# Performance work log

Hardware: AMD Instinct MI355X
Metric: run time of the kernel (lower is better)

The kernel has to match this reference:

```python
import jax, jax.numpy as jnp
import numpy as np

B, T, C = 2, 2048, 1024
NH = 16
HD = C // NH

def build_alibi_bias(n_head, max_len):
    slopes = jnp.arange(1, n_head + 1, dtype=jnp.float32) / n_head  # [nh]
    ar = jnp.arange(max_len, dtype=jnp.float32)
    # bias[h, i, j] = slopes[h] * (j - i)
    return slopes[:, None, None] * (ar[None, None, :] - ar[None, :, None])

def setup_inputs() -> dict:
    key = jax.random.key(0)
    ks = jax.random.split(key, 7)
    s = 0.02
    return {
        "x": jax.random.normal(ks[0], (B, T, C), dtype=jnp.float32),
        "q_w": jax.random.normal(ks[1], (C, C), dtype=jnp.float32) * s,   # [in, out]
        "q_b": jnp.zeros((C,), dtype=jnp.float32),
        "kv_w": jax.random.normal(ks[2], (C, 2 * C), dtype=jnp.float32) * s,
        "kv_b": jnp.zeros((2 * C,), dtype=jnp.float32),
        "o_w": jax.random.normal(ks[3], (C, C), dtype=jnp.float32) * s,
        "o_b": jnp.zeros((C,), dtype=jnp.float32),
    }

def reference(x, q_w, q_b, kv_w, kv_b, o_w, o_b):
    Bx, Tx, Cx = x.shape
    q = (x @ q_w + q_b).reshape(Bx, Tx, NH, HD).transpose(0, 2, 1, 3)      # [B,nh,T,hd]
    kv = (x @ kv_w + kv_b).reshape(Bx, Tx, 2, NH, HD).transpose(2, 0, 3, 1, 4)
    k, v = kv[0], kv[1]                                                     # [B,nh,T,hd]
    att = jnp.einsum("bhqd,bhkd->bhqk", q, k) * (1.0 / np.sqrt(HD))        # [B,nh,T,T]
    att = att + build_alibi_bias(NH, Tx)[None]                              # ALiBi bias
    causal = jnp.tril(jnp.ones((Tx, Tx), dtype=bool))
    att = jnp.where(causal[None, None], att, -jnp.inf)
    att = jax.nn.softmax(att, axis=-1)
    y = jnp.einsum("bhqk,bhkd->bhqd", att, v)                               # [B,nh,T,hd]
    y = y.transpose(0, 2, 1, 3).reshape(Bx, Tx, Cx)
    return y @ o_w + o_b
```

## Files before the change

kernel.cpp:

```cpp
#include <hip/hip_runtime.h>
#include <hip/hip_bf16.h>

#define NB 2
#define NT 2048
#define NC 1024
#define NHD 16
#define HDD 64
#define LOG2E 1.4426950408889634f

typedef __attribute__((ext_vector_type(8))) short short8;
typedef __attribute__((ext_vector_type(4))) short short4v;
typedef __attribute__((ext_vector_type(4))) float f32x4;
typedef __attribute__((ext_vector_type(16))) float f32x16;

__device__ __forceinline__ ushort f2bf(float f) {
    union { float f; unsigned u; } v; v.f = f;
    unsigned u = v.u;
    unsigned r = (u + 0x7FFFu + ((u >> 16) & 1u)) >> 16;
    return (ushort)r;
}

__device__ __forceinline__ float bf2f(ushort u) {
    unsigned x = ((unsigned)u) << 16;
    float f; __builtin_memcpy(&f, &x, 4); return f;
}

__device__ __forceinline__ unsigned pkbf(float a, float b) {
    __hip_bfloat162 t = __float22bfloat162_rn(float2{a, b});
    unsigned u; __builtin_memcpy(&u, &t, 4); return u;
}

__device__ __forceinline__ void gload16(const ushort* g, ushort* l) {
    __builtin_amdgcn_global_load_lds((const __attribute__((address_space(1))) void*)g,
                                     (__attribute__((address_space(3))) void*)l, 16, 0, 0);
}

__device__ __forceinline__ void tcvt_tile(const float* __restrict__ src, ushort* __restrict__ dst,
                                          int Kd, int Nd, int kb, int nb)
{
    __shared__ ushort tile[64][68];
    const int tid = threadIdx.x;
    const int r = tid >> 2, c = (tid & 3) * 16;
    const float* sp = src + (size_t)(kb + r) * Nd + nb + c;
#pragma unroll
    for (int i = 0; i < 16; i += 4) {
        float4 v = *(const float4*)(sp + i);
        tile[r][c + i + 0] = f2bf(v.x);
        tile[r][c + i + 1] = f2bf(v.y);
        tile[r][c + i + 2] = f2bf(v.z);
        tile[r][c + i + 3] = f2bf(v.w);
    }
    __syncthreads();
    ushort* dp = dst + (size_t)(nb + r) * Kd + kb + c;
#pragma unroll
    for (int i = 0; i < 16; i += 8) {
        short8 o;
#pragma unroll
        for (int j = 0; j < 8; j++) o[j] = (short)tile[c + i + j][r];
        *(short8*)(dp + i) = o;
    }
}

__global__ __launch_bounds__(256)
void prep(const float* __restrict__ x, const float* __restrict__ q_w,
          const float* __restrict__ kv_w, const float* __restrict__ o_w,
          ushort* __restrict__ xb, ushort* __restrict__ wqkvT, ushort* __restrict__ woT)
{
    const int bid = blockIdx.x;
    if (bid < 2048) {
        int i = (bid * 256 + threadIdx.x) * 8;
        float4 a = *(const float4*)(x + i);
        float4 b = *(const float4*)(x + i + 4);
        short8 o;
        o[0] = (short)f2bf(a.x); o[1] = (short)f2bf(a.y);
        o[2] = (short)f2bf(a.z); o[3] = (short)f2bf(a.w);
        o[4] = (short)f2bf(b.x); o[5] = (short)f2bf(b.y);
        o[6] = (short)f2bf(b.z); o[7] = (short)f2bf(b.w);
        *(short8*)(xb + i) = o;
    } else if (bid < 2304) {
        int r = bid - 2048;
        tcvt_tile(q_w, wqkvT, 1024, 1024, (r & 15) * 64, (r >> 4) * 64);
    } else if (bid < 2816) {
        int r = bid - 2304;
        tcvt_tile(kv_w, wqkvT + 1024 * 1024, 1024, 2048, (r & 15) * 64, (r >> 4) * 64);
    } else {
        int r = bid - 2816;
        tcvt_tile(o_w, woT, 1024, 1024, (r & 15) * 64, (r >> 4) * 64);
    }
}

template<int MODE>
__global__ __launch_bounds__(256)
void gemm128(const ushort* __restrict__ A, const ushort* __restrict__ Bt,
             const float* __restrict__ bias0, const float* __restrict__ bias1,
             ushort* __restrict__ Qo, ushort* __restrict__ Ko, ushort* __restrict__ VoT,
             float* __restrict__ Fo, int Kdim)
{
    __shared__ ushort Al[2][128 * 32];
    __shared__ ushort Bl[2][128 * 32];
    const int tid = threadIdx.x;
    const int lane = tid & 63, w = tid >> 6;
    const int wr = (w >> 1) * 64, wc = (w & 1) * 64;
    const int lg = lane >> 4, lc = lane & 15;

    const int nwg = gridDim.x;
    const int cpx = nwg >> 3;
    const int sid = (blockIdx.x & 7) * cpx + (blockIdx.x >> 3);
    const int bm = (sid & 31) * 128, bn = (sid >> 5) * 128;

    f32x4 acc[4][4] = {};

    const int srow = lane >> 2, scol = (lane & 3) * 8;
    const int seg0 = w * 2;

    const ushort* apb = A  + (size_t)(bm + seg0 * 16 + srow) * Kdim + scol;
    const ushort* bpb = Bt + (size_t)(bn + seg0 * 16 + srow) * Kdim + scol;

    gload16(apb,              &Al[0][seg0 * 512]);
    gload16(apb + 16 * Kdim,  &Al[0][(seg0 + 1) * 512]);
    gload16(bpb,              &Bl[0][seg0 * 512]);
    gload16(bpb + 16 * Kdim,  &Bl[0][(seg0 + 1) * 512]);

    int cur = 0;
    for (int k0 = 0; k0 < Kdim; k0 += 32) {
        __syncthreads();
        if (k0 + 32 < Kdim) {
            gload16(apb + (k0 + 32),             &Al[cur ^ 1][seg0 * 512]);
            gload16(apb + (k0 + 32) + 16 * Kdim, &Al[cur ^ 1][(seg0 + 1) * 512]);
            gload16(bpb + (k0 + 32),             &Bl[cur ^ 1][seg0 * 512]);
            gload16(bpb + (k0 + 32) + 16 * Kdim, &Bl[cur ^ 1][(seg0 + 1) * 512]);
        }
        short8 af[4], bfv[4];
#pragma unroll
        for (int mt = 0; mt < 4; mt++) af[mt] = *(const short8*)&Al[cur][(wr + mt*16 + lc) * 32 + lg*8];
#pragma unroll
        for (int nt = 0; nt < 4; nt++) bfv[nt] = *(const short8*)&Bl[cur][(wc + nt*16 + lc) * 32 + lg*8];
        __builtin_amdgcn_s_setprio(1);
#pragma unroll
        for (int mt = 0; mt < 4; mt++)
#pragma unroll
            for (int nt = 0; nt < 4; nt++)
                acc[mt][nt] = __builtin_amdgcn_mfma_f32_16x16x32_bf16(af[mt], bfv[nt], acc[mt][nt], 0, 0, 0);
        __builtin_amdgcn_s_setprio(0);
        cur ^= 1;
    }

#pragma unroll
    for (int mt = 0; mt < 4; mt++) {
#pragma unroll
        for (int nt = 0; nt < 4; nt++) {
            const int n = bn + wc + nt * 16 + lc;
            const int mb = bm + wr + mt * 16 + lg * 4;
            if (MODE == 1) {
#pragma unroll
                for (int rr = 0; rr < 4; rr++)
                    Fo[(size_t)(mb + rr) * NC + n] = acc[mt][nt][rr] + bias0[n];
            } else {
                const int b = mb >> 11, t = mb & 2047;
                const int reg = n >> 10;
                if (reg == 0) {
                    int hh = n >> 6, d = n & 63;
                    ushort* qp = Qo + (((size_t)b * NHD + hh) * NT + t) * HDD + d;
#pragma unroll
                    for (int rr = 0; rr < 4; rr++)
                        qp[rr * HDD] = f2bf((acc[mt][nt][rr] + bias0[n]) * (0.125f * LOG2E));
                } else if (reg == 1) {
                    int j = n - NC;
                    int hh = j >> 6, d = j & 63;
                    ushort* kp = Ko + (((size_t)b * NHD + hh) * NT + t) * HDD + d;
#pragma unroll
                    for (int rr = 0; rr < 4; rr++)
                        kp[rr * HDD] = f2bf(acc[mt][nt][rr] + bias1[j]);
                } else {
                    int j = n - NC;
                    int jj = j - 1024;
                    int hh = jj >> 6, d = jj & 63;
                    short4v o;
#pragma unroll
                    for (int rr = 0; rr < 4; rr++)
                        o[rr] = (short)f2bf(acc[mt][nt][rr] + bias1[j]);
                    *(short4v*)&VoT[(((size_t)b * NHD + hh) * HDD + d) * NT + t] = o;
                }
            }
        }
    }
}

__global__ __launch_bounds__(256, 3)
void attn_fwd(const ushort* __restrict__ Q, const ushort* __restrict__ K,
              const ushort* __restrict__ Vt, ushort* __restrict__ Y,
              ushort* __restrict__ pool0, ushort* __restrict__ pool1,
              float* __restrict__ mlb)
{
    __shared__ ushort sb[2 * 2 * 64 * 72];

    const int tid = threadIdx.x;
    const int lane = tid & 63, w = tid >> 6;
    const int lo5 = lane & 31, hi = lane >> 5;
    const int slot = (int)(blockIdx.x >> 5);
    const int bh = blockIdx.x & 31;
    const int b = bh >> 4, h = bh & 15;

    int qt, seg, nseg;
    if (slot < 16)      { qt = 15 - (slot >> 2); seg = slot & 3; nseg = 4; }
    else if (slot < 28) { int u = slot - 16; int q3 = u / 3; qt = 11 - q3; seg = u - q3 * 3; nseg = 3; }
    else if (slot < 36) { int u = slot - 28; qt = 7 - (u >> 1); seg = u & 1; nseg = 2; }
    else                { qt = 39 - slot; seg = 0; nseg = 1; }
    const int T = 2 * qt + 2;
    const int t_begin = (seg * T) / nseg;
    const int t_end   = ((seg + 1) * T) / nseg;
    const bool split = (nseg > 1);
    int pi = 0;
    if (split) {
        int pbase = (qt < 8) ? (qt - 4) * 2 : ((qt < 12) ? 8 + (qt - 8) * 3 : 20 + (qt - 12) * 4);
        pi = bh * 36 + pbase + seg;
    }

    const ushort* Qp = Q + (size_t)bh * NT * HDD;
    const ushort* Kp = K + (size_t)bh * NT * HDD;
    const ushort* Vp = Vt + (size_t)bh * HDD * NT;

    const int q0 = qt * 128 + w * 32;
    const int qlane = q0 + lo5;

    const float slope2 = (float)(h + 1) * (LOG2E / (float)NHD);

    short8 qf[4];
    {
        const ushort* qr = Qp + (size_t)qlane * HDD + 8 * hi;
#pragma unroll
        for (int kk = 0; kk < 4; kk++) qf[kk] = *(const short8*)(qr + kk * 16);
    }

    short8 ones;
#pragma unroll
    for (int j = 0; j < 8; j++) ones[j] = (short)0x3F80;

    float bb[16];
#pragma unroll
    for (int r = 0; r < 16; r++) {
        int roff = (r & 3) + 8 * (r >> 2) + 4 * hi;
        bb[r] = slope2 * ((float)roff - (float)qlane);
    }

    float m_s = -1e30f, l_s = 0.f;
    f32x16 accO[2] = {};

    const int sr = tid >> 2, sd = (tid & 3) * 16;

    short8 pk0, pk1, pv0, pv1;
    {
        const ushort* kp = Kp + (size_t)(t_begin * 64 + sr) * HDD + sd;
        pk0 = *(const short8*)kp;
        pk1 = *(const short8*)(kp + 8);
        const ushort* vp = Vp + (size_t)sr * NT + t_begin * 64 + sd;
        pv0 = *(const short8*)vp;
        pv1 = *(const short8*)(vp + 8);
    }

    for (int t = t_begin; t < t_end; t++) {
        const int kv0 = t * 64;
        ushort* Kl = sb + ((t - t_begin) & 1) * 2 * 64 * 72;
        ushort* Vl = Kl + 64 * 72;
        *(short8*)&Kl[sr * 72 + sd]     = pk0;
        *(short8*)&Kl[sr * 72 + sd + 8] = pk1;
        *(short8*)&Vl[sr * 72 + sd]     = pv0;
        *(short8*)&Vl[sr * 72 + sd + 8] = pv1;
        __syncthreads();

        if (t + 1 < t_end) {
            const int kv1 = kv0 + 64;
            const ushort* kp = Kp + (size_t)(kv1 + sr) * HDD + sd;
            pk0 = *(const short8*)kp;
            pk1 = *(const short8*)(kp + 8);
            const ushort* vp = Vp + (size_t)sr * NT + kv1 + sd;
            pv0 = *(const short8*)vp;
            pv1 = *(const short8*)(vp + 8);
        }

#pragma unroll
        for (int sub = 0; sub < 2; sub++) {
            const int kv0s = kv0 + sub * 32;
            if (kv0s > q0 + 31) continue;

            f32x16 S = {};
            __builtin_amdgcn_s_setprio(1);
#pragma unroll
            for (int kk = 0; kk < 4; kk++) {
                short8 kf = *(const short8*)&Kl[(sub * 32 + lo5) * 72 + kk * 16 + 8 * hi];
                S = __builtin_amdgcn_mfma_f32_32x32x16_bf16(kf, qf[kk], S, 0, 0, 0);
            }
            __builtin_amdgcn_s_setprio(0);

            const float sk = slope2 * (float)kv0s;
            float mloc = m_s - sk;

            if (kv0s + 31 > q0) {
#pragma unroll
                for (int r = 0; r < 16; r++) {
                    int kvr = kv0s + (r & 3) + 8 * (r >> 2) + 4 * hi;
                    S[r] = (kvr > qlane) ? -1e30f : (S[r] + bb[r]);
                }
            } else {
#pragma unroll
                for (int r = 0; r < 16; r++) S[r] = S[r] + bb[r];
            }

            float a0 = fmaxf(fmaxf(S[0], S[1]), S[2]);
            float a1 = fmaxf(fmaxf(S[3], S[4]), S[5]);
            float a2 = fmaxf(fmaxf(S[6], S[7]), S[8]);
            float a3 = fmaxf(fmaxf(S[9], S[10]), S[11]);
            float a4 = fmaxf(fmaxf(S[12], S[13]), S[14]);
            float rmax = fmaxf(fmaxf(fmaxf(a0, a1), fmaxf(a2, a3)), fmaxf(a4, S[15]));
            rmax = fmaxf(rmax, __shfl_xor(rmax, 32));

            if (__any(rmax - mloc > 8.0f)) {
                float mn = fmaxf(mloc, rmax);
                float sc = __builtin_amdgcn_exp2f(mloc - mn);
                mloc = mn;
                l_s *= sc;
#pragma unroll
                for (int dt = 0; dt < 2; dt++)
#pragma unroll
                    for (int r = 0; r < 16; r++) accO[dt][r] *= sc;
            }
            m_s = mloc + sk;

#pragma unroll
            for (int r = 0; r < 16; r++)
                S[r] = __builtin_amdgcn_exp2f(S[r] - mloc);

            unsigned pw[8], px[8];
#pragma unroll
            for (int i = 0; i < 8; i++) pw[i] = pkbf(S[2 * i], S[2 * i + 1]);
#pragma unroll
            for (int i = 0; i < 8; i++) px[i] = __shfl_xor(pw[i], 32);
            union { unsigned u[4]; short8 s; } fa0, fa1;
            fa0.u[0] = hi ? px[2] : pw[0];
            fa0.u[1] = hi ? px[3] : pw[1];
            fa0.u[2] = hi ? pw[2] : px[0];
            fa0.u[3] = hi ? pw[3] : px[1];
            fa1.u[0] = hi ? px[6] : pw[4];
            fa1.u[1] = hi ? px[7] : pw[5];
            fa1.u[2] = hi ? pw[6] : px[4];
            fa1.u[3] = hi ? pw[7] : px[5];

            f32x16 z = {};
            __builtin_amdgcn_s_setprio(1);
            z = __builtin_amdgcn_mfma_f32_32x32x16_bf16(ones, fa0.s, z, 0, 0, 0);
            z = __builtin_amdgcn_mfma_f32_32x32x16_bf16(ones, fa1.s, z, 0, 0, 0);

#pragma unroll
            for (int dt = 0; dt < 2; dt++) {
                short8 vf0 = *(const short8*)&Vl[(dt * 32 + lo5) * 72 + sub * 32 + 8 * hi];
                short8 vf1 = *(const short8*)&Vl[(dt * 32 + lo5) * 72 + sub * 32 + 16 + 8 * hi];
                accO[dt] = __builtin_amdgcn_mfma_f32_32x32x16_bf16(vf0, fa0.s, accO[dt], 0, 0, 0);
                accO[dt] = __builtin_amdgcn_mfma_f32_32x32x16_bf16(vf1, fa1.s, accO[dt], 0, 0, 0);
            }
            __builtin_amdgcn_s_setprio(0);

            l_s += z[0];
        }
    }

    const float invl = split ? 1.0f : __builtin_amdgcn_rcpf(l_s);
    __syncthreads();
    ushort* myO = sb + w * 32 * 72;
#pragma unroll
    for (int dt = 0; dt < 2; dt++)
#pragma unroll
        for (int r = 0; r < 16; r++) {
            int d = dt * 32 + (r & 3) + 8 * (r >> 2) + 4 * hi;
            myO[lo5 * 72 + d] = f2bf(accO[dt][r] * invl);
        }
    if (split && hi == 0) {
        int rowin = w * 32 + lo5;
        mlb[pi * 256 + rowin] = m_s;
        mlb[pi * 256 + 128 + rowin] = l_s;
    }
    __syncthreads();
    const int orow = lane >> 1, ocol = (lane & 1) * 32;
    if (split) {
        ushort* pp = (pi < 320 ? pool0 + (size_t)pi * 8192 : pool1 + (size_t)(pi - 320) * 8192)
                     + (w * 32 + orow) * 64 + ocol;
#pragma unroll
        for (int c = 0; c < 4; c++)
            *(short8*)(pp + c * 8) = *(const short8*)&myO[orow * 72 + ocol + c * 8];
    } else {
        ushort* yp = Y + ((size_t)b * NT + q0 + orow) * NC + h * HDD + ocol;
#pragma unroll
        for (int c = 0; c < 4; c++)
            *(short8*)(yp + c * 8) = *(const short8*)&myO[orow * 72 + ocol + c * 8];
    }
}

__global__ __launch_bounds__(256)
void combine(const ushort* __restrict__ pool0, const ushort* __restrict__ pool1,
             const float* __restrict__ mlb, ushort* __restrict__ Y)
{
    const int cb = blockIdx.x;
    const int bh = cb / 12, qs = cb % 12;
    const int qt = qs + 4;
    const int b = bh >> 4, h = bh & 15;
    const int nseg = (qs < 4) ? 2 : ((qs < 8) ? 3 : 4);
    const int pbase = (qs < 4) ? qs * 2 : ((qs < 8) ? 8 + (qs - 4) * 3 : 20 + (qs - 8) * 4);
    const int pi0 = bh * 36 + pbase;

    const int tid = threadIdx.x;
    const int r = tid >> 1, c0 = (tid & 1) * 32;

    float m[4], l[4], a[4];
    float M = -1e30f;
    for (int s = 0; s < nseg; s++) {
        m[s] = mlb[(pi0 + s) * 256 + r];
        l[s] = mlb[(pi0 + s) * 256 + 128 + r];
        M = fmaxf(M, m[s]);
    }
    float L = 0.f;
    for (int s = 0; s < nseg; s++) { a[s] = __builtin_amdgcn_exp2f(m[s] - M); L += a[s] * l[s]; }
    const float inv = __builtin_amdgcn_rcpf(L);

    const ushort* pp[4];
    for (int s = 0; s < nseg; s++) {
        int pi = pi0 + s;
        pp[s] = (pi < 320 ? pool0 + (size_t)pi * 8192 : pool1 + (size_t)(pi - 320) * 8192) + r * 64 + c0;
    }
    ushort* yp = Y + ((size_t)b * NT + qt * 128 + r) * NC + h * HDD + c0;

#pragma unroll
    for (int c = 0; c < 4; c++) {
        float acc[8] = {};
        for (int s = 0; s < nseg; s++) {
            short8 u = *(const short8*)(pp[s] + c * 8);
#pragma unroll
            for (int j = 0; j < 8; j++) acc[j] += a[s] * bf2f((ushort)u[j]);
        }
        short8 o;
#pragma unroll
        for (int j = 0; j < 8; j++) o[j] = (short)f2bf(acc[j] * inv);
        *(short8*)(yp + c * 8) = o;
    }
}

extern "C" void kernel_launch(void* const* d_in, const int* in_sizes, int n_in,
                              void* d_out, int out_size, void* d_ws, size_t ws_size,
                              hipStream_t stream)
{
    const float* x    = (const float*)d_in[0];
    const float* q_w  = (const float*)d_in[1];
    const float* q_b  = (const float*)d_in[2];
    const float* kv_w = (const float*)d_in[3];
    const float* kv_b = (const float*)d_in[4];
    const float* o_w  = (const float*)d_in[5];
    const float* o_b  = (const float*)d_in[6];
    float* out = (float*)d_out;

    char* ws = (char*)d_ws;
    ushort* xb    = (ushort*)(ws);
    ushort* wqkvT = (ushort*)(ws + 8388608);
    ushort* woT   = (ushort*)(ws + 14680064);
    ushort* Qs    = (ushort*)(ws + 16777216);
    ushort* Ks    = (ushort*)(ws + 25165824);
    ushort* VsT   = (ushort*)(ws + 33554432);
    ushort* Ys    = (ushort*)(ws + 41943040);
    ushort* pool0 = wqkvT;
    ushort* pool1 = (ushort*)out;
    float*  mlb   = (float*)((char*)out + 832 * 16384);

    prep<<<3072, 256, 0, stream>>>(x, q_w, kv_w, o_w, xb, wqkvT, woT);
    gemm128<0><<<768, 256, 0, stream>>>(xb, wqkvT, q_b, kv_b, Qs, Ks, VsT, nullptr, 1024);
    attn_fwd<<<1280, 256, 0, stream>>>(Qs, Ks, VsT, Ys, pool0, pool1, mlb);
    combine<<<384, 256, 0, stream>>>(pool0, pool1, mlb, Ys);
    gemm128<1><<<256, 256, 0, stream>>>(Ys, woT, o_b, nullptr, nullptr, nullptr, nullptr, out, 1024);
}
```

Measured before the change: 132.9 us.

## Triple-buffer GEMM K-loop and use permlane32 swap for P fragment

The projection GEMM moves from double to triple-buffered LDS staging. It prefetches two K-steps ahead and uses explicit vmcnt waits plus a single barrier per iteration in place of __syncthreads. Separately, the attention kernel replaces eight cross-half shuffles and selects with four v_permlane32_swap instructions to build the bf16 P operand. This is meant to hide global-load latency and cut shuffle cost, at the price of extra LDS per block and a reliance on the swap semantics matching the old layout.

```diff
diff --git a/kernel.cpp b/kernel.cpp
--- a/kernel.cpp
+++ b/kernel.cpp
@@ -96,8 +96,8 @@
              ushort* __restrict__ Qo, ushort* __restrict__ Ko, ushort* __restrict__ VoT,
              float* __restrict__ Fo, int Kdim)
 {
-    __shared__ ushort Al[2][128 * 32];
-    __shared__ ushort Bl[2][128 * 32];
+    __shared__ ushort Al[3][128 * 32];
+    __shared__ ushort Bl[3][128 * 32];
     const int tid = threadIdx.x;
     const int lane = tid & 63, w = tid >> 6;
     const int wr = (w >> 1) * 64, wc = (w & 1) * 64;
@@ -116,19 +116,24 @@
     const ushort* apb = A  + (size_t)(bm + seg0 * 16 + srow) * Kdim + scol;
     const ushort* bpb = Bt + (size_t)(bn + seg0 * 16 + srow) * Kdim + scol;
 
-    gload16(apb,              &Al[0][seg0 * 512]);
-    gload16(apb + 16 * Kdim,  &Al[0][(seg0 + 1) * 512]);
-    gload16(bpb,              &Bl[0][seg0 * 512]);
-    gload16(bpb + 16 * Kdim,  &Bl[0][(seg0 + 1) * 512]);
+#define STAGE(K0, BUF)                                            \
+    do {                                                          \
+        gload16(apb + (K0),             &Al[BUF][seg0 * 512]);    \
+        gload16(apb + (K0) + 16 * Kdim, &Al[BUF][(seg0 + 1) * 512]); \
+        gload16(bpb + (K0),             &Bl[BUF][seg0 * 512]);    \
+        gload16(bpb + (K0) + 16 * Kdim, &Bl[BUF][(seg0 + 1) * 512]); \
+    } while (0)
+
+    STAGE(0, 0);
+    STAGE(32, 1);
+    asm volatile("s_waitcnt vmcnt(4) lgkmcnt(0)" ::: "memory");
+    __builtin_amdgcn_s_barrier();
 
     int cur = 0;
     for (int k0 = 0; k0 < Kdim; k0 += 32) {
-        __syncthreads();
-        if (k0 + 32 < Kdim) {
-            gload16(apb + (k0 + 32),             &Al[cur ^ 1][seg0 * 512]);
-            gload16(apb + (k0 + 32) + 16 * Kdim, &Al[cur ^ 1][(seg0 + 1) * 512]);
-            gload16(bpb + (k0 + 32),             &Bl[cur ^ 1][seg0 * 512]);
-            gload16(bpb + (k0 + 32) + 16 * Kdim, &Bl[cur ^ 1][(seg0 + 1) * 512]);
+        if (k0 + 64 < Kdim) {
+            int nxt2 = cur == 0 ? 2 : cur - 1;
+            STAGE(k0 + 64, nxt2);
         }
         short8 af[4], bfv[4];
 #pragma unroll
@@ -142,8 +147,16 @@
             for (int nt = 0; nt < 4; nt++)
                 acc[mt][nt] = __builtin_amdgcn_mfma_f32_16x16x32_bf16(af[mt], bfv[nt], acc[mt][nt], 0, 0, 0);
         __builtin_amdgcn_s_setprio(0);
-        cur ^= 1;
-    }
+        if (k0 + 32 < Kdim) {
+            if (k0 + 64 < Kdim)
+                asm volatile("s_waitcnt vmcnt(4) lgkmcnt(0)" ::: "memory");
+            else
+                asm volatile("s_waitcnt vmcnt(0) lgkmcnt(0)" ::: "memory");
+            __builtin_amdgcn_s_barrier();
+        }
+        cur = (cur == 2) ? 0 : cur + 1;
+    }
+#undef STAGE
 
 #pragma unroll
     for (int mt = 0; mt < 4; mt++) {
@@ -330,20 +343,16 @@
             for (int r = 0; r < 16; r++)
                 S[r] = __builtin_amdgcn_exp2f(S[r] - mloc);
 
-            unsigned pw[8], px[8];
+            unsigned pw[8];
 #pragma unroll
             for (int i = 0; i < 8; i++) pw[i] = pkbf(S[2 * i], S[2 * i + 1]);
-#pragma unroll
-            for (int i = 0; i < 8; i++) px[i] = __shfl_xor(pw[i], 32);
+            asm volatile("v_permlane32_swap_b32 %0, %1" : "+v"(pw[0]), "+v"(pw[2]));
+            asm volatile("v_permlane32_swap_b32 %0, %1" : "+v"(pw[1]), "+v"(pw[3]));
+            asm volatile("v_permlane32_swap_b32 %0, %1" : "+v"(pw[4]), "+v"(pw[6]));
+            asm volatile("v_permlane32_swap_b32 %0, %1" : "+v"(pw[5]), "+v"(pw[7]));
             union { unsigned u[4]; short8 s; } fa0, fa1;
-            fa0.u[0] = hi ? px[2] : pw[0];
-            fa0.u[1] = hi ? px[3] : pw[1];
-            fa0.u[2] = hi ? pw[2] : px[0];
-            fa0.u[3] = hi ? pw[3] : px[1];
-            fa1.u[0] = hi ? px[6] : pw[4];
-            fa1.u[1] = hi ? px[7] : pw[5];
-            fa1.u[2] = hi ? pw[6] : px[4];
-            fa1.u[3] = hi ? pw[7] : px[5];
+            fa0.u[0] = pw[0]; fa0.u[1] = pw[1]; fa0.u[2] = pw[2]; fa0.u[3] = pw[3];
+            fa1.u[0] = pw[4]; fa1.u[1] = pw[5]; fa1.u[2] = pw[6]; fa1.u[3] = pw[7];
 
             f32x16 z = {};
             __builtin_amdgcn_s_setprio(1);
```

Result: slower. 174.7 us (+31.5%).
